# Kernel optimization log

Hardware: AMD Instinct MI355X
Metric: run time of the kernel (lower is better)

## Reference

```python
import jax, jax.numpy as jnp
import numpy as np

D_MODEL = 1024
HEADS = 16
D_HEAD = D_MODEL // HEADS


def setup_inputs() -> dict:
    key = jax.random.key(0)
    ks = jax.random.split(key, 7)
    s = 1.0 / np.sqrt(D_MODEL)
    x = jax.random.normal(ks[0], (4, 2048, D_MODEL), dtype=jnp.float32)
    Wq = jax.random.uniform(ks[1], (D_MODEL, D_MODEL), jnp.float32, -s, s)
    bq = jax.random.uniform(ks[2], (D_MODEL,), jnp.float32, -s, s)
    Wk = jax.random.uniform(ks[3], (D_MODEL, D_MODEL), jnp.float32, -s, s)
    bk = jax.random.uniform(ks[4], (D_MODEL,), jnp.float32, -s, s)
    Wv = jax.random.uniform(ks[5], (D_MODEL, D_MODEL), jnp.float32, -s, s)
    bv = jax.random.uniform(ks[6], (D_MODEL,), jnp.float32, -s, s)
    return {"x": x, "Wq": Wq, "bq": bq, "Wk": Wk, "bk": bk, "Wv": Wv, "bv": bv}


def reference(x, Wq, bq, Wk, bk, Wv, bv):
    B, S, D = x.shape
    # QKV projections, split heads: [B, H, S, Dh]
    def split(t):
        return t.reshape(B, S, HEADS, D_HEAD).transpose(0, 2, 1, 3)
    q = split(x @ Wq + bq)
    k = split(x @ Wk + bk)
    v = split(x @ Wv + bv)
    scores = jnp.einsum('bhqd,bhkd->bhqk', q, k) / np.sqrt(D_HEAD).astype(jnp.float32)
    attn = jax.nn.softmax(scores, axis=-1)
    out = jnp.einsum('bhqk,bhkd->bhqd', attn, v)
    return out.transpose(0, 2, 1, 3).reshape(B, S, D)
```

## Files before the change

### kernel.cpp

```cpp
#include <hip/hip_runtime.h>

typedef _Float16 f16;
typedef __attribute__((ext_vector_type(2))) _Float16 f16x2;
typedef __attribute__((ext_vector_type(2))) __fp16   hf16x2;
typedef __attribute__((ext_vector_type(4))) _Float16 f16x4;
typedef __attribute__((ext_vector_type(8))) _Float16 f16x8;
typedef __attribute__((ext_vector_type(4))) float    f32x4;

#define D_MODEL 1024
#define HEADS   16
#define DH      64
#define SEQ     2048
#define BATCH   4
#define SSCALE  0.1803368801111204f

__device__ __forceinline__ void gload_lds16(const void* g, void* lds) {
  __builtin_amdgcn_global_load_lds(
      (const __attribute__((address_space(1))) unsigned int*)g,
      (__attribute__((address_space(3))) unsigned int*)lds, 16, 0, 0);
}

__global__ __launch_bounds__(256) void prep_kernel(const float* __restrict__ x,
                                                   const float* __restrict__ Wq,
                                                   const float* __restrict__ Wk,
                                                   const float* __restrict__ Wv,
                                                   f16* __restrict__ xb,
                                                   f16* __restrict__ wt) {
  if (blockIdx.x < 8192) {
    int i = blockIdx.x * 256 + threadIdx.x;
    float4 v = ((const float4*)x)[i];
    f16x4 h;
    h[0] = (f16)v.x; h[1] = (f16)v.y; h[2] = (f16)v.z; h[3] = (f16)v.w;
    ((f16x4*)xb)[i] = h;
    return;
  }
  int bid = blockIdx.x - 8192;
  int z = bid >> 8, rem = bid & 255;
  const float* W = z == 0 ? Wq : (z == 1 ? Wk : Wv);
  f16* out = wt + (size_t)z * D_MODEL * D_MODEL;
  __shared__ float tile[64][65];
  int n0 = (rem & 15) * 64, k0 = (rem >> 4) * 64;
  int tx = threadIdx.x & 63, ty = threadIdx.x >> 6;
#pragma unroll
  for (int r = 0; r < 16; ++r)
    tile[ty * 16 + r][tx] = W[(size_t)(k0 + ty * 16 + r) * D_MODEL + n0 + tx];
  __syncthreads();
#pragma unroll
  for (int r = 0; r < 16; ++r)
    out[(size_t)(n0 + ty * 16 + r) * D_MODEL + k0 + tx] = (f16)tile[tx][ty * 16 + r];
}

__global__ __launch_bounds__(256, 3) void qkv_gemm_kernel(
    const f16* __restrict__ xb, const f16* __restrict__ wt_all,
    const float* __restrict__ bq, const float* __restrict__ bk, const float* __restrict__ bv,
    f16* __restrict__ qout, f16* __restrict__ kout, f16* __restrict__ vtout) {
  const int bid = blockIdx.x;
  const int j = bid & 7, t = bid >> 3;
  const int by = j * 8 + (t & 7);
  const int bx = (t >> 3) & 7;
  const int z  = t >> 6;
  const f16* wt = wt_all + (size_t)z * D_MODEL * D_MODEL;
  const float* bias = z == 0 ? bq : (z == 1 ? bk : bv);
  const int n0 = bx * 128, m0 = by * 128;

  __shared__ f16 As[3][128 * 32];
  __shared__ f16 Bs[3][128 * 32];

  const int tid = threadIdx.x;
  const int lane = tid & 63, w = tid >> 6;
  const int quad = lane >> 4, l15 = lane & 15;
  const int wm = w & 1, wn = w >> 1;

  const int pce = (quad ^ ((l15 >> 1) & 3)) * 8;
  const int aoff = wm * 2048 + l15 * 32 + pce;
  const int boff = wn * 2048 + l15 * 32 + pce;

  int srow[2], scl[2];
#pragma unroll
  for (int c = 0; c < 2; ++c) {
    int slot = (w * 2 + c) * 64 + lane;
    srow[c] = slot >> 2;
    scl[c] = (slot & 3) ^ ((srow[c] >> 1) & 3);
  }

  f32x4 acc[4][4];
#pragma unroll
  for (int i = 0; i < 4; ++i)
#pragma unroll
    for (int jj = 0; jj < 4; ++jj) acc[i][jj] = (f32x4){0.f, 0.f, 0.f, 0.f};

#pragma unroll
  for (int tt = 0; tt < 2; ++tt)
#pragma unroll
    for (int c = 0; c < 2; ++c) {
      gload_lds16(xb + (size_t)(m0 + srow[c]) * D_MODEL + tt * 32 + scl[c] * 8, &As[tt][(w * 2 + c) * 512]);
      gload_lds16(wt + (size_t)(n0 + srow[c]) * D_MODEL + tt * 32 + scl[c] * 8, &Bs[tt][(w * 2 + c) * 512]);
    }

  f16x8 aP[4], bP[4];
  int buf = 0;
  for (int it = 0; it < 32; ++it) {
    if (it == 31) { asm volatile("s_waitcnt vmcnt(0)" ::: "memory"); }
    else          { asm volatile("s_waitcnt vmcnt(4)" ::: "memory"); }
    __builtin_amdgcn_s_barrier();
    __builtin_amdgcn_sched_barrier(0);
    if (it < 30) {
      const int sb = buf ? buf - 1 : 2;
      const int kn = (it + 2) * 32;
#pragma unroll
      for (int c = 0; c < 2; ++c) {
        gload_lds16(xb + (size_t)(m0 + srow[c]) * D_MODEL + kn + scl[c] * 8, &As[sb][(w * 2 + c) * 512]);
        gload_lds16(wt + (size_t)(n0 + srow[c]) * D_MODEL + kn + scl[c] * 8, &Bs[sb][(w * 2 + c) * 512]);
      }
    }
    f16x8 aC[4], bC[4];
#pragma unroll
    for (int mt = 0; mt < 4; ++mt) aC[mt] = *(const f16x8*)(&As[buf][aoff + mt * 512]);
#pragma unroll
    for (int nt = 0; nt < 4; ++nt) bC[nt] = *(const f16x8*)(&Bs[buf][boff + nt * 512]);
    if (it) {
#pragma unroll
      for (int mt = 0; mt < 4; ++mt)
#pragma unroll
        for (int nt = 0; nt < 4; ++nt)
          acc[mt][nt] = __builtin_amdgcn_mfma_f32_16x16x32_f16(aP[mt], bP[nt], acc[mt][nt], 0, 0, 0);
    }
#pragma unroll
    for (int tt = 0; tt < 4; ++tt) { aP[tt] = aC[tt]; bP[tt] = bC[tt]; }
    buf = (buf == 2) ? 0 : buf + 1;
  }
#pragma unroll
  for (int mt = 0; mt < 4; ++mt)
#pragma unroll
    for (int nt = 0; nt < 4; ++nt)
      acc[mt][nt] = __builtin_amdgcn_mfma_f32_16x16x32_f16(aP[mt], bP[nt], acc[mt][nt], 0, 0, 0);

  const float sc = (z == 0) ? SSCALE : 1.0f;
  float bcol[4];
#pragma unroll
  for (int nt = 0; nt < 4; ++nt) bcol[nt] = bias[n0 + wn * 64 + nt * 16 + l15];

  if (z < 2) {
    f16* out = (z == 0) ? qout : kout;
#pragma unroll
    for (int mt = 0; mt < 4; ++mt) {
      int mbase = m0 + wm * 64 + mt * 16 + quad * 4;
#pragma unroll
      for (int nt = 0; nt < 4; ++nt) {
        int n = n0 + wn * 64 + nt * 16 + l15;
        int h = n >> 6, dh = n & 63;
#pragma unroll
        for (int r = 0; r < 4; ++r) {
          int m = mbase + r;
          int b = m >> 11, s = m & 2047;
          out[((size_t)(b * HEADS + h) * SEQ + s) * DH + dh] = (f16)((acc[mt][nt][r] + bcol[nt]) * sc);
        }
      }
    }
  } else {
#pragma unroll
    for (int mt = 0; mt < 4; ++mt) {
      int mbase = m0 + wm * 64 + mt * 16 + quad * 4;
      int b = mbase >> 11, seq = mbase & 2047;
      int kt = seq >> 6;
#pragma unroll
      for (int nt = 0; nt < 4; ++nt) {
        int n = n0 + wn * 64 + nt * 16 + l15;
        int h = n >> 6, dh = n & 63;
        f16x4 v;
#pragma unroll
        for (int r = 0; r < 4; ++r) v[r] = (f16)(acc[mt][nt][r] + bcol[nt]);
        int phys = (quad * 2 + (mt >> 1)) ^ (dh & 7);
        size_t off = (((size_t)(b * HEADS + h) * 32 + kt) * 4096) + dh * 64 + phys * 8 + (mt & 1) * 4;
        *(f16x4*)(vtout + off) = v;
      }
    }
  }
}

__global__ __launch_bounds__(128, 2) void attn_kernel(
    const f16* __restrict__ q, const f16* __restrict__ k, const f16* __restrict__ vt,
    float* __restrict__ out) {
  const int bh = blockIdx.x;
  const int s0 = blockIdx.y * 128;
  const int b = bh >> 4, h = bh & 15;
  const int tid = threadIdx.x, lane = tid & 63, w = tid >> 6;
  const int quad = lane >> 4, l15 = lane & 15;

  __shared__ f16 Ks[2][64 * 64];
  __shared__ f16 Vs[2][64 * 64];

  const f16* qbase = q + ((size_t)bh * SEQ + s0 + w * 64) * DH;
  const f16* kbase = k + (size_t)bh * SEQ * DH;
  const f16* vbase = vt + (size_t)bh * DH * SEQ;

  f16x8 qf[4][2];
#pragma unroll
  for (int qt = 0; qt < 4; ++qt)
#pragma unroll
    for (int ks = 0; ks < 2; ++ks)
      qf[qt][ks] = *(const f16x8*)(qbase + (qt * 16 + l15) * DH + ks * 32 + quad * 8);

  int koff[2];
  koff[0] = l15 * 64 + ((quad ^ (l15 & 7)) * 8);
  koff[1] = l15 * 64 + (((4 + quad) ^ (l15 & 7)) * 8);
  int voff2[2];
  voff2[0] = l15 * 64 + (((quad * 2) ^ (l15 & 7)) * 8);
  voff2[1] = l15 * 64 + (((quad * 2 + 1) ^ (l15 & 7)) * 8);

  int srow[4], scl[4];
#pragma unroll
  for (int c = 0; c < 4; ++c) {
    int slot = (w * 4 + c) * 64 + lane;
    srow[c] = slot >> 3;
    scl[c] = (slot & 7) ^ (srow[c] & 7);
  }
  int vslot[4];
#pragma unroll
  for (int c = 0; c < 4; ++c) vslot[c] = ((w * 4 + c) * 64 + lane) * 8;

  f32x4 lsum4[4];
#pragma unroll
  for (int qt = 0; qt < 4; ++qt) lsum4[qt] = (f32x4){0.f, 0.f, 0.f, 0.f};
  f32x4 o[4][4];
#pragma unroll
  for (int i = 0; i < 4; ++i)
#pragma unroll
    for (int jj = 0; jj < 4; ++jj) o[i][jj] = (f32x4){0.f, 0.f, 0.f, 0.f};
  const f32x4 Zero = (f32x4){0.f, 0.f, 0.f, 0.f};

#pragma unroll
  for (int c = 0; c < 4; ++c)
    gload_lds16(kbase + (size_t)srow[c] * DH + scl[c] * 8, &Ks[0][(w * 4 + c) * 512]);
#pragma unroll
  for (int c = 0; c < 4; ++c)
    gload_lds16(vbase + vslot[c], &Vs[0][(w * 4 + c) * 512]);

  for (int kt = 0; kt < SEQ / 64; ++kt) {
    const int buf = kt & 1;
    __syncthreads();
    if (kt < SEQ / 64 - 1) {
      const int kn = (kt + 1) * 64;
#pragma unroll
      for (int c = 0; c < 4; ++c)
        gload_lds16(kbase + (size_t)(kn + srow[c]) * DH + scl[c] * 8, &Ks[buf ^ 1][(w * 4 + c) * 512]);
#pragma unroll
      for (int c = 0; c < 4; ++c)
        gload_lds16(vbase + (kt + 1) * 4096 + vslot[c], &Vs[buf ^ 1][(w * 4 + c) * 512]);
    }

    f32x4 st[4][4];
#pragma unroll
    for (int mt = 0; mt < 4; ++mt) {
      f16x8 af0 = *(const f16x8*)(&Ks[buf][koff[0] + mt * 1024]);
      f16x8 af1 = *(const f16x8*)(&Ks[buf][koff[1] + mt * 1024]);
#pragma unroll
      for (int qt = 0; qt < 4; ++qt) {
        st[mt][qt] = __builtin_amdgcn_mfma_f32_16x16x32_f16(af0, qf[qt][0], Zero, 0, 0, 0);
        st[mt][qt] = __builtin_amdgcn_mfma_f32_16x16x32_f16(af1, qf[qt][1], st[mt][qt], 0, 0, 0);
      }
    }

    f16x4 pb[4][4];
#pragma unroll
    for (int ks = 0; ks < 4; ++ks)
#pragma unroll
      for (int qt = 0; qt < 4; ++qt) {
        float e0 = __builtin_amdgcn_exp2f(st[ks][qt][0]);
        float e1 = __builtin_amdgcn_exp2f(st[ks][qt][1]);
        float e2 = __builtin_amdgcn_exp2f(st[ks][qt][2]);
        float e3 = __builtin_amdgcn_exp2f(st[ks][qt][3]);
        f32x4 ev = (f32x4){e0, e1, e2, e3};
        lsum4[qt] += ev;
        f16x2 p01 = __builtin_bit_cast(f16x2, __builtin_amdgcn_cvt_pkrtz(e0, e1));
        f16x2 p23 = __builtin_bit_cast(f16x2, __builtin_amdgcn_cvt_pkrtz(e2, e3));
        pb[ks][qt] = __builtin_shufflevector(p01, p23, 0, 1, 2, 3);
      }

#pragma unroll
    for (int half = 0; half < 2; ++half)
#pragma unroll
      for (int mt = 0; mt < 4; ++mt) {
        f16x8 v8 = *(const f16x8*)(&Vs[buf][voff2[half] + mt * 1024]);
        f16x4 vaA = __builtin_shufflevector(v8, v8, 0, 1, 2, 3);
        f16x4 vaB = __builtin_shufflevector(v8, v8, 4, 5, 6, 7);
#pragma unroll
        for (int qt = 0; qt < 4; ++qt) {
          o[mt][qt] = __builtin_amdgcn_mfma_f32_16x16x16f16(vaA, pb[half * 2][qt], o[mt][qt], 0, 0, 0);
          o[mt][qt] = __builtin_amdgcn_mfma_f32_16x16x16f16(vaB, pb[half * 2 + 1][qt], o[mt][qt], 0, 0, 0);
        }
      }
  }

#pragma unroll
  for (int qt = 0; qt < 4; ++qt) {
    float l = (lsum4[qt][0] + lsum4[qt][1]) + (lsum4[qt][2] + lsum4[qt][3]);
    l += __shfl_xor(l, 16, 64);
    l += __shfl_xor(l, 32, 64);
    float inv = 1.f / l;
    int sq = s0 + w * 64 + qt * 16 + l15;
    float* obase = out + ((size_t)b * SEQ + sq) * D_MODEL + h * DH;
#pragma unroll
    for (int mt = 0; mt < 4; ++mt) {
      f32x4 vv;
#pragma unroll
      for (int r = 0; r < 4; ++r) vv[r] = o[mt][qt][r] * inv;
      *(f32x4*)(obase + mt * 16 + quad * 4) = vv;
    }
  }
}

extern "C" void kernel_launch(void* const* d_in, const int* in_sizes, int n_in,
                              void* d_out, int out_size, void* d_ws, size_t ws_size,
                              hipStream_t stream) {
  const float* x  = (const float*)d_in[0];
  const float* Wq = (const float*)d_in[1];
  const float* bq = (const float*)d_in[2];
  const float* Wk = (const float*)d_in[3];
  const float* bk = (const float*)d_in[4];
  const float* Wv = (const float*)d_in[5];
  const float* bv = (const float*)d_in[6];
  float* out = (float*)d_out;

  char* ws = (char*)d_ws;
  f16* xb = (f16*)ws;
  f16* wt = (f16*)(ws + (size_t)16 * 1024 * 1024);
  f16* q  = (f16*)(ws + (size_t)22 * 1024 * 1024);
  f16* kk = q + (size_t)BATCH * SEQ * D_MODEL;
  f16* vt = kk + (size_t)BATCH * SEQ * D_MODEL;

  prep_kernel<<<8192 + 768, 256, 0, stream>>>(x, Wq, Wk, Wv, xb, wt);
  qkv_gemm_kernel<<<1536, 256, 0, stream>>>(xb, wt, bq, bk, bv, q, kk, vt);
  attn_kernel<<<dim3(64, 16), 128, 0, stream>>>(q, kk, vt, out);
}
```

Measured before the change: 244.4 us.

## Switch attention MFMAs to 32x32x16 tiles with permlane32 swap for P operand

Rewrites the attention inner loop to use 32x32x16 f16 MFMA instructions for both QK^T and PV instead of 16x16 variants. Softmax probabilities are repacked into B-operand layout with v_permlane32_swap, avoiding an LDS round trip. The V-transpose layout written by the projection kernel is changed to match the new fragment access pattern. This is meant to cut instruction count and LDS reads per FLOP, in exchange for larger accumulator register footprint and more complex lane mapping.

```diff
diff --git a/kernel.cpp b/kernel.cpp
--- a/kernel.cpp
+++ b/kernel.cpp
@@ -6,6 +6,8 @@
 typedef __attribute__((ext_vector_type(4))) _Float16 f16x4;
 typedef __attribute__((ext_vector_type(8))) _Float16 f16x8;
 typedef __attribute__((ext_vector_type(4))) float    f32x4;
+typedef __attribute__((ext_vector_type(16))) float   f32x16;
+typedef __attribute__((ext_vector_type(4))) unsigned u32x4;
 
 #define D_MODEL 1024
 #define HEADS   16
@@ -170,8 +172,8 @@
         f16x4 v;
 #pragma unroll
         for (int r = 0; r < 4; ++r) v[r] = (f16)(acc[mt][nt][r] + bcol[nt]);
-        int phys = (quad * 2 + (mt >> 1)) ^ (dh & 7);
-        size_t off = (((size_t)(b * HEADS + h) * 32 + kt) * 4096) + dh * 64 + phys * 8 + (mt & 1) * 4;
+        int phys = (mt * 2 + (quad >> 1)) ^ (dh & 7);
+        size_t off = (((size_t)(b * HEADS + h) * 32 + kt) * 4096) + dh * 64 + phys * 8 + (quad & 1) * 4;
         *(f16x4*)(vtout + off) = v;
       }
     }
@@ -185,28 +187,20 @@
   const int s0 = blockIdx.y * 128;
   const int b = bh >> 4, h = bh & 15;
   const int tid = threadIdx.x, lane = tid & 63, w = tid >> 6;
-  const int quad = lane >> 4, l15 = lane & 15;
+  const int l31 = lane & 31, hi = lane >> 5;
 
   __shared__ f16 Ks[2][64 * 64];
   __shared__ f16 Vs[2][64 * 64];
 
-  const f16* qbase = q + ((size_t)bh * SEQ + s0 + w * 64) * DH;
   const f16* kbase = k + (size_t)bh * SEQ * DH;
   const f16* vbase = vt + (size_t)bh * DH * SEQ;
 
-  f16x8 qf[4][2];
-#pragma unroll
-  for (int qt = 0; qt < 4; ++qt)
-#pragma unroll
-    for (int ks = 0; ks < 2; ++ks)
-      qf[qt][ks] = *(const f16x8*)(qbase + (qt * 16 + l15) * DH + ks * 32 + quad * 8);
-
-  int koff[2];
-  koff[0] = l15 * 64 + ((quad ^ (l15 & 7)) * 8);
-  koff[1] = l15 * 64 + (((4 + quad) ^ (l15 & 7)) * 8);
-  int voff2[2];
-  voff2[0] = l15 * 64 + (((quad * 2) ^ (l15 & 7)) * 8);
-  voff2[1] = l15 * 64 + (((quad * 2 + 1) ^ (l15 & 7)) * 8);
+  f16x8 qg[2][4];
+#pragma unroll
+  for (int qh = 0; qh < 2; ++qh)
+#pragma unroll
+    for (int ks = 0; ks < 4; ++ks)
+      qg[qh][ks] = *(const f16x8*)(q + ((size_t)bh * SEQ + s0 + w * 64 + qh * 32 + l31) * DH + ks * 16 + hi * 8);
 
   int srow[4], scl[4];
 #pragma unroll
@@ -219,15 +213,17 @@
 #pragma unroll
   for (int c = 0; c < 4; ++c) vslot[c] = ((w * 4 + c) * 64 + lane) * 8;
 
-  f32x4 lsum4[4];
-#pragma unroll
-  for (int qt = 0; qt < 4; ++qt) lsum4[qt] = (f32x4){0.f, 0.f, 0.f, 0.f};
-  f32x4 o[4][4];
-#pragma unroll
-  for (int i = 0; i < 4; ++i)
-#pragma unroll
-    for (int jj = 0; jj < 4; ++jj) o[i][jj] = (f32x4){0.f, 0.f, 0.f, 0.f};
-  const f32x4 Zero = (f32x4){0.f, 0.f, 0.f, 0.f};
+  float lsum[2] = {0.f, 0.f};
+  f32x16 o[2][2];
+#pragma unroll
+  for (int i = 0; i < 2; ++i)
+#pragma unroll
+    for (int jj = 0; jj < 2; ++jj)
+#pragma unroll
+      for (int e = 0; e < 16; ++e) o[i][jj][e] = 0.f;
+  f32x16 Zero;
+#pragma unroll
+  for (int e = 0; e < 16; ++e) Zero[e] = 0.f;
 
 #pragma unroll
   for (int c = 0; c < 4; ++c)
@@ -249,64 +245,78 @@
         gload_lds16(vbase + (kt + 1) * 4096 + vslot[c], &Vs[buf ^ 1][(w * 4 + c) * 512]);
     }
 
-    f32x4 st[4][4];
-#pragma unroll
-    for (int mt = 0; mt < 4; ++mt) {
-      f16x8 af0 = *(const f16x8*)(&Ks[buf][koff[0] + mt * 1024]);
-      f16x8 af1 = *(const f16x8*)(&Ks[buf][koff[1] + mt * 1024]);
-#pragma unroll
-      for (int qt = 0; qt < 4; ++qt) {
-        st[mt][qt] = __builtin_amdgcn_mfma_f32_16x16x32_f16(af0, qf[qt][0], Zero, 0, 0, 0);
-        st[mt][qt] = __builtin_amdgcn_mfma_f32_16x16x32_f16(af1, qf[qt][1], st[mt][qt], 0, 0, 0);
-      }
-    }
-
-    f16x4 pb[4][4];
-#pragma unroll
-    for (int ks = 0; ks < 4; ++ks)
-#pragma unroll
-      for (int qt = 0; qt < 4; ++qt) {
-        float e0 = __builtin_amdgcn_exp2f(st[ks][qt][0]);
-        float e1 = __builtin_amdgcn_exp2f(st[ks][qt][1]);
-        float e2 = __builtin_amdgcn_exp2f(st[ks][qt][2]);
-        float e3 = __builtin_amdgcn_exp2f(st[ks][qt][3]);
-        f32x4 ev = (f32x4){e0, e1, e2, e3};
-        lsum4[qt] += ev;
-        f16x2 p01 = __builtin_bit_cast(f16x2, __builtin_amdgcn_cvt_pkrtz(e0, e1));
-        f16x2 p23 = __builtin_bit_cast(f16x2, __builtin_amdgcn_cvt_pkrtz(e2, e3));
-        pb[ks][qt] = __builtin_shufflevector(p01, p23, 0, 1, 2, 3);
-      }
-
-#pragma unroll
-    for (int half = 0; half < 2; ++half)
-#pragma unroll
-      for (int mt = 0; mt < 4; ++mt) {
-        f16x8 v8 = *(const f16x8*)(&Vs[buf][voff2[half] + mt * 1024]);
-        f16x4 vaA = __builtin_shufflevector(v8, v8, 0, 1, 2, 3);
-        f16x4 vaB = __builtin_shufflevector(v8, v8, 4, 5, 6, 7);
-#pragma unroll
-        for (int qt = 0; qt < 4; ++qt) {
-          o[mt][qt] = __builtin_amdgcn_mfma_f32_16x16x16f16(vaA, pb[half * 2][qt], o[mt][qt], 0, 0, 0);
-          o[mt][qt] = __builtin_amdgcn_mfma_f32_16x16x16f16(vaB, pb[half * 2 + 1][qt], o[mt][qt], 0, 0, 0);
+#pragma unroll
+    for (int skh = 0; skh < 2; ++skh) {
+      const int krow = skh * 32 + l31;
+      const int krx = krow & 7;
+      f32x16 st0 = Zero, st1 = Zero;
+#pragma unroll
+      for (int ks = 0; ks < 4; ++ks) {
+        f16x8 a = *(const f16x8*)(&Ks[buf][krow * 64 + (((ks << 1) | hi) ^ krx) * 8]);
+        st0 = __builtin_amdgcn_mfma_f32_32x32x16_f16(a, qg[0][ks], st0, 0, 0, 0);
+        st1 = __builtin_amdgcn_mfma_f32_32x32x16_f16(a, qg[1][ks], st1, 0, 0, 0);
+      }
+
+      f16x8 bop[2][2];
+#pragma unroll
+      for (int qh = 0; qh < 2; ++qh) {
+        const f32x16 stv = qh ? st1 : st0;
+        unsigned d0, d1, d2, d3, d4, d5, d6, d7;
+        float e0, e1, acc = 0.f;
+        e0 = __builtin_amdgcn_exp2f(stv[0]);  e1 = __builtin_amdgcn_exp2f(stv[1]);
+        acc += e0 + e1; d0 = __builtin_bit_cast(unsigned, __builtin_amdgcn_cvt_pkrtz(e0, e1));
+        e0 = __builtin_amdgcn_exp2f(stv[2]);  e1 = __builtin_amdgcn_exp2f(stv[3]);
+        acc += e0 + e1; d1 = __builtin_bit_cast(unsigned, __builtin_amdgcn_cvt_pkrtz(e0, e1));
+        e0 = __builtin_amdgcn_exp2f(stv[4]);  e1 = __builtin_amdgcn_exp2f(stv[5]);
+        acc += e0 + e1; d2 = __builtin_bit_cast(unsigned, __builtin_amdgcn_cvt_pkrtz(e0, e1));
+        e0 = __builtin_amdgcn_exp2f(stv[6]);  e1 = __builtin_amdgcn_exp2f(stv[7]);
+        acc += e0 + e1; d3 = __builtin_bit_cast(unsigned, __builtin_amdgcn_cvt_pkrtz(e0, e1));
+        e0 = __builtin_amdgcn_exp2f(stv[8]);  e1 = __builtin_amdgcn_exp2f(stv[9]);
+        acc += e0 + e1; d4 = __builtin_bit_cast(unsigned, __builtin_amdgcn_cvt_pkrtz(e0, e1));
+        e0 = __builtin_amdgcn_exp2f(stv[10]); e1 = __builtin_amdgcn_exp2f(stv[11]);
+        acc += e0 + e1; d5 = __builtin_bit_cast(unsigned, __builtin_amdgcn_cvt_pkrtz(e0, e1));
+        e0 = __builtin_amdgcn_exp2f(stv[12]); e1 = __builtin_amdgcn_exp2f(stv[13]);
+        acc += e0 + e1; d6 = __builtin_bit_cast(unsigned, __builtin_amdgcn_cvt_pkrtz(e0, e1));
+        e0 = __builtin_amdgcn_exp2f(stv[14]); e1 = __builtin_amdgcn_exp2f(stv[15]);
+        acc += e0 + e1; d7 = __builtin_bit_cast(unsigned, __builtin_amdgcn_cvt_pkrtz(e0, e1));
+        lsum[qh] += acc;
+        asm("v_permlane32_swap_b32 %0, %1" : "+v"(d0), "+v"(d2));
+        asm("v_permlane32_swap_b32 %0, %1" : "+v"(d1), "+v"(d3));
+        asm("v_permlane32_swap_b32 %0, %1" : "+v"(d4), "+v"(d6));
+        asm("v_permlane32_swap_b32 %0, %1" : "+v"(d5), "+v"(d7));
+        bop[0][qh] = __builtin_bit_cast(f16x8, (u32x4){d0, d1, d2, d3});
+        bop[1][qh] = __builtin_bit_cast(f16x8, (u32x4){d4, d5, d6, d7});
+      }
+
+#pragma unroll
+      for (int ks16 = 0; ks16 < 2; ++ks16) {
+#pragma unroll
+        for (int dhh = 0; dhh < 2; ++dhh) {
+          const int vrow = dhh * 32 + l31;
+          f16x8 va = *(const f16x8*)(&Vs[buf][vrow * 64 + (((skh * 4 + ks16 * 2 + hi) ^ (vrow & 7)) * 8)]);
+          o[dhh][0] = __builtin_amdgcn_mfma_f32_32x32x16_f16(va, bop[ks16][0], o[dhh][0], 0, 0, 0);
+          o[dhh][1] = __builtin_amdgcn_mfma_f32_32x32x16_f16(va, bop[ks16][1], o[dhh][1], 0, 0, 0);
         }
       }
-  }
-
-#pragma unroll
-  for (int qt = 0; qt < 4; ++qt) {
-    float l = (lsum4[qt][0] + lsum4[qt][1]) + (lsum4[qt][2] + lsum4[qt][3]);
-    l += __shfl_xor(l, 16, 64);
+    }
+  }
+
+#pragma unroll
+  for (int qh = 0; qh < 2; ++qh) {
+    float l = lsum[qh];
     l += __shfl_xor(l, 32, 64);
     float inv = 1.f / l;
-    int sq = s0 + w * 64 + qt * 16 + l15;
+    int sq = s0 + w * 64 + qh * 32 + l31;
     float* obase = out + ((size_t)b * SEQ + sq) * D_MODEL + h * DH;
 #pragma unroll
-    for (int mt = 0; mt < 4; ++mt) {
-      f32x4 vv;
-#pragma unroll
-      for (int r = 0; r < 4; ++r) vv[r] = o[mt][qt][r] * inv;
-      *(f32x4*)(obase + mt * 16 + quad * 4) = vv;
-    }
+    for (int dhh = 0; dhh < 2; ++dhh)
+#pragma unroll
+      for (int g = 0; g < 4; ++g) {
+        f32x4 vv;
+#pragma unroll
+        for (int r = 0; r < 4; ++r) vv[r] = o[dhh][qh][g * 4 + r] * inv;
+        *(f32x4*)(obase + dhh * 32 + g * 8 + hi * 4) = vv;
+      }
   }
 }
 
```

Result: no change. 239.7 us (-1.9%).
